# Optimization experiments

Measured on AMD Instinct MI355X. Metric: run time of the kernel, lower is better.

The kernel has to match this reference:

```python
import jax, jax.numpy as jnp
import numpy as np

B, S, D, E, K = 4, 4096, 2048, 64, 2


def setup_inputs() -> dict:
    key = jax.random.key(0)
    kx, kwg, kwn, kn = jax.random.split(key, 4)
    scale = 1.0 / np.sqrt(D)
    return {
        "x": jax.random.normal(kx, (B, S, D), dtype=jnp.float32),
        "Wg": jax.random.normal(kwg, (E, D), dtype=jnp.float32) * scale,
        "bg": jnp.zeros((E,), dtype=jnp.float32),
        "Wn": jax.random.normal(kwn, (E, D), dtype=jnp.float32) * scale,
        "bn": jnp.zeros((E,), dtype=jnp.float32),
        "noise": jax.random.normal(kn, (B, S, E), dtype=jnp.float32),
    }


def reference(x, Wg, bg, Wn, bn, noise):
    # gate / noise projections: [B,S,D] @ [D,E] -> [B,S,E]
    gate_logits = jnp.einsum("bsd,ed->bse", x, Wg) + bg
    noise_std = jax.nn.softplus(jnp.einsum("bsd,ed->bse", x, Wn) + bn)
    noisy_logits = gate_logits + noise * noise_std  # training-mode path

    # top-k over experts, then scatter back with -inf elsewhere
    flat = noisy_logits.reshape(-1, E)  # [T, E], T = B*S
    top_vals, top_idx = jax.lax.top_k(flat, K)  # [T, K]
    T = flat.shape[0]
    neg_inf = jnp.full((T, E), -jnp.inf, dtype=flat.dtype)
    full_logits = neg_inf.at[jnp.arange(T)[:, None], top_idx].set(top_vals)

    gate_probs = jax.nn.softmax(full_logits, axis=-1).reshape(B, S, E)
    top_k_indices = top_idx.reshape(B, S, K)
    return gate_probs, top_k_indices
```

## Files before the change

### kernel.cpp

```cpp
#include <hip/hip_runtime.h>
#include <math.h>
#include <stdint.h>

#define D_ 2048
#define E_ 64
#define T_ 16384

#define BM 32
#define BK 32
#define KTILES 64
#define ABUF_B 4096
#define BBUF_B 16384
#define BUF_B (ABUF_B + BBUF_B)
#define CT_STRIDE 132

typedef _Float16 h8 __attribute__((ext_vector_type(8)));
typedef float f4v __attribute__((ext_vector_type(4)));

__device__ __forceinline__ void split2(const float4& a, const float4& b,
                                       h8& h, h8& m) {
    const float xe[8] = {a.x, a.y, a.z, a.w, b.x, b.y, b.z, b.w};
#pragma unroll
    for (int i = 0; i < 8; ++i) {
        const _Float16 hh_ = (_Float16)xe[i];
        const float r = (xe[i] - (float)hh_) * 1024.0f;
        h[i] = hh_;
        m[i] = (_Float16)r;
    }
}

__device__ __forceinline__ void gload16(const void* g, void* l) {
    __builtin_amdgcn_global_load_lds(
        (const __attribute__((address_space(1))) uint32_t*)g,
        (__attribute__((address_space(3))) uint32_t*)l, 16, 0, 0);
}

__device__ __forceinline__ void topk_epilogue(float g, float nl, float nz,
                                              int lane, size_t tg,
                                              float* __restrict__ out_probs,
                                              float* __restrict__ out_idx) {
    const float sp = fmaxf(nl, 0.f) + log1pf(expf(-fabsf(nl)));
    const float noisy = g + nz * sp;

    float v = noisy;
    int idx = lane;
#pragma unroll
    for (int off = 32; off > 0; off >>= 1) {
        const float ov = __shfl_xor(v, off);
        const int oi = __shfl_xor(idx, off);
        if (ov > v || (ov == v && oi < idx)) { v = ov; idx = oi; }
    }
    const float v1 = v;
    const int i1 = idx;
    v = (lane == i1) ? -INFINITY : noisy;
    idx = lane;
#pragma unroll
    for (int off = 32; off > 0; off >>= 1) {
        const float ov = __shfl_xor(v, off);
        const int oi = __shfl_xor(idx, off);
        if (ov > v || (ov == v && oi < idx)) { v = ov; idx = oi; }
    }
    const float v2 = v;
    const int i2 = idx;

    const float e2 = expf(v2 - v1);
    const float denom = 1.f + e2;
    const float p = (lane == i1) ? (1.f / denom)
                                 : ((lane == i2) ? (e2 / denom) : 0.f);
    out_probs[tg * E_ + lane] = p;
    if (lane == 0) {
        out_idx[tg * 2 + 0] = (float)i1;
        out_idx[tg * 2 + 1] = (float)i2;
    }
}

__global__ void w_split_kernel(const float* __restrict__ Wg,
                               const float* __restrict__ Wn,
                               h8* __restrict__ wsp) {
    const int idx = blockIdx.x * blockDim.x + threadIdx.x;
    const int lane = idx & 63;
    const int s = (idx >> 6) & 63;
    const int f = idx >> 12;
    const int n = f * 16 + (lane & 15);
    const int k0 = s * 32 + ((lane >> 4) << 3);
    const float* src = (n < 64) ? &Wg[(size_t)n * D_ + k0]
                                : &Wn[(size_t)(n - 64) * D_ + k0];
    h8 hv, mv;
#pragma unroll
    for (int i = 0; i < 8; ++i) {
        const float w = src[i];
        const _Float16 wh = (_Float16)w;
        const float r = (w - (float)wh) * 1024.0f;
        hv[i] = wh;
        mv[i] = (_Float16)r;
    }
    wsp[0 * 32768 + idx] = hv;
    wsp[1 * 32768 + idx] = mv;
}

__launch_bounds__(512)
__global__ void gemm_topk_kernel(const float* __restrict__ x,
                                 const h8* __restrict__ wsp,
                                 const float* __restrict__ bg,
                                 const float* __restrict__ bn,
                                 const float* __restrict__ noise,
                                 float* __restrict__ out_probs,
                                 float* __restrict__ out_idx) {
    __shared__ __align__(16) char smem[2 * BUF_B];
    const int tid = threadIdx.x;
    const int lane = tid & 63;
    const int wv = tid >> 6;
    const int wm = wv >> 2;
    const int wn = wv & 3;
    const int block_m0 = blockIdx.x * BM;

    const int arow = lane & 15;
    const int akg = lane >> 4;
    const char* wb = (const char*)wsp;

    f4v hh0{}, hh1{}, hm0{}, hm1{}, mh0{}, mh1{}, mm0{}, mm1{};

    const int sar = tid >> 3;
    const int sac = tid & 7;
    const float* sasrc = x + (size_t)(block_m0 + sar) * D_ + ((sac ^ (sar & 7)) << 2);
    const int blv = lane;

    auto STAGE = [&](int t, int b) {
        char* base = smem + b * BUF_B;
        if (tid < 256)
            gload16(sasrc + t * BK, base + tid * 16);
        gload16(wb + ((size_t)(0 * 32768 + wv * 4096 + t * 64 + blv)) * 16,
                base + ABUF_B + ((0 * 8 + wv) * 64 + blv) * 16);
        gload16(wb + ((size_t)(1 * 32768 + wv * 4096 + t * 64 + blv)) * 16,
                base + ABUF_B + ((1 * 8 + wv) * 64 + blv) * 16);
    };

    auto COMPUTE = [&](int b) {
        const char* base = smem + b * BUF_B;
        const int r = wm * 16 + arow;
        const int swz = r & 7;
        const float4 f0 = *(const float4*)(base + r * 128 + (((akg * 2 + 0) ^ swz) << 4));
        const float4 f1 = *(const float4*)(base + r * 128 + (((akg * 2 + 1) ^ swz) << 4));
        h8 xh, xm;
        split2(f0, f1, xh, xm);
        const char* Bb = base + ABUF_B;
        const int fA = wn * 2, fB = wn * 2 + 1;
        const h8 bh0 = *(const h8*)(Bb + (fA * 64 + lane) * 16);
        const h8 bh1 = *(const h8*)(Bb + (fB * 64 + lane) * 16);
        const h8 bm0 = *(const h8*)(Bb + ((8 + fA) * 64 + lane) * 16);
        const h8 bm1 = *(const h8*)(Bb + ((8 + fB) * 64 + lane) * 16);
#define MF(A, B, C) C = __builtin_amdgcn_mfma_f32_16x16x32_f16(A, B, C, 0, 0, 0)
        MF(xh, bh0, hh0); MF(xh, bh1, hh1);
        MF(xh, bm0, hm0); MF(xh, bm1, hm1);
        MF(xm, bh0, mh0); MF(xm, bh1, mh1);
        MF(xm, bm0, mm0); MF(xm, bm1, mm1);
#undef MF
    };

    STAGE(0, 0);
    __syncthreads();
    int cur = 0;
#pragma unroll 1
    for (int t = 0; t < KTILES; ++t) {
        if (t + 1 < KTILES) STAGE(t + 1, cur ^ 1);
        COMPUTE(cur);
        __syncthreads();
        cur ^= 1;
    }

    float* Ct = (float*)smem;
    {
        const float S1 = 1.0f / 1024.0f;
        const float S2 = S1 * S1;
        const int ko4 = akg * 4;
#pragma unroll
        for (int r = 0; r < 4; ++r) {
            const int row = wm * 16 + ko4 + r;
            const int col0 = (wn * 2 + 0) * 16 + arow;
            const int col1 = (wn * 2 + 1) * 16 + arow;
            Ct[row * CT_STRIDE + col0] = hh0[r] + (hm0[r] + mh0[r]) * S1 + mm0[r] * S2;
            Ct[row * CT_STRIDE + col1] = hh1[r] + (hm1[r] + mh1[r]) * S1 + mm1[r] * S2;
        }
    }
    __syncthreads();

    const float my_bg = bg[lane];
    const float my_bn = bn[lane];
#pragma unroll 1
    for (int tt = 0; tt < 4; ++tt) {
        const int tl = wv * 4 + tt;
        const size_t tg = (size_t)block_m0 + tl;
        const float g = Ct[tl * CT_STRIDE + lane] + my_bg;
        const float nl = Ct[tl * CT_STRIDE + 64 + lane] + my_bn;
        const float nz = noise[tg * E_ + lane];
        topk_epilogue(g, nl, nz, lane, tg, out_probs, out_idx);
    }
}

#define FBM 64
#define FBK 32
#define XS_STRIDE 68
#define WS_STRIDE 132
#define FCT_STRIDE 132

__launch_bounds__(256)
__global__ void noisy_topk_f32_kernel(const float* __restrict__ x,
                                      const float* __restrict__ Wg,
                                      const float* __restrict__ bg,
                                      const float* __restrict__ Wn,
                                      const float* __restrict__ bn,
                                      const float* __restrict__ noise,
                                      float* __restrict__ out_probs,
                                      float* __restrict__ out_idx) {
    __shared__ float smem[FBM * FCT_STRIDE];
    float* Xs = smem;
    float* Ws = smem + FBK * XS_STRIDE;

    const int tid = threadIdx.x;
    const int block_m0 = blockIdx.x * FBM;
    const int n0 = (tid & 31) * 4;
    const int m0 = (tid >> 5) * 8;

    float acc[8][4];
#pragma unroll
    for (int i = 0; i < 8; ++i)
#pragma unroll
        for (int j = 0; j < 4; ++j) acc[i][j] = 0.f;

    const int sj = tid & 7;
    const int sr = tid >> 3;

    for (int k0 = 0; k0 < D_; k0 += FBK) {
        __syncthreads();
#pragma unroll
        for (int it = 0; it < 2; ++it) {
            const int m = sr + it * 32;
            const float4 v = *reinterpret_cast<const float4*>(
                &x[(size_t)(block_m0 + m) * D_ + k0 + 4 * sj]);
            Xs[(4 * sj + 0) * XS_STRIDE + m] = v.x;
            Xs[(4 * sj + 1) * XS_STRIDE + m] = v.y;
            Xs[(4 * sj + 2) * XS_STRIDE + m] = v.z;
            Xs[(4 * sj + 3) * XS_STRIDE + m] = v.w;
        }
#pragma unroll
        for (int it = 0; it < 4; ++it) {
            const int n = sr + it * 32;
            const float* wrow = (n < 64) ? &Wg[(size_t)n * D_] : &Wn[(size_t)(n - 64) * D_];
            const float4 v = *reinterpret_cast<const float4*>(&wrow[k0 + 4 * sj]);
            Ws[(4 * sj + 0) * WS_STRIDE + n] = v.x;
            Ws[(4 * sj + 1) * WS_STRIDE + n] = v.y;
            Ws[(4 * sj + 2) * WS_STRIDE + n] = v.z;
            Ws[(4 * sj + 3) * WS_STRIDE + n] = v.w;
        }
        __syncthreads();
#pragma unroll
        for (int k = 0; k < FBK; ++k) {
            const float4 a0 = *reinterpret_cast<const float4*>(&Xs[k * XS_STRIDE + m0]);
            const float4 a1 = *reinterpret_cast<const float4*>(&Xs[k * XS_STRIDE + m0 + 4]);
            const float4 b4 = *reinterpret_cast<const float4*>(&Ws[k * WS_STRIDE + n0]);
            const float am[8] = {a0.x, a0.y, a0.z, a0.w, a1.x, a1.y, a1.z, a1.w};
            const float bb[4] = {b4.x, b4.y, b4.z, b4.w};
#pragma unroll
            for (int i = 0; i < 8; ++i)
#pragma unroll
                for (int j = 0; j < 4; ++j)
                    acc[i][j] = fmaf(am[i], bb[j], acc[i][j]);
        }
    }

    __syncthreads();
    float* Ct = smem;
#pragma unroll
    for (int i = 0; i < 8; ++i)
#pragma unroll
        for (int j = 0; j < 4; ++j)
            Ct[(m0 + i) * FCT_STRIDE + n0 + j] = acc[i][j];
    __syncthreads();

    const int wave = tid >> 6;
    const int lane = tid & 63;
    const float my_bg = bg[lane];
    const float my_bn = bn[lane];
#pragma unroll 1
    for (int tt = 0; tt < 16; ++tt) {
        const int tl = wave * 16 + tt;
        const size_t tg = (size_t)block_m0 + tl;
        const float g = Ct[tl * FCT_STRIDE + lane] + my_bg;
        const float nl = Ct[tl * FCT_STRIDE + 64 + lane] + my_bn;
        const float nz = noise[tg * E_ + lane];
        topk_epilogue(g, nl, nz, lane, tg, out_probs, out_idx);
    }
}

extern "C" void kernel_launch(void* const* d_in, const int* in_sizes, int n_in,
                              void* d_out, int out_size, void* d_ws, size_t ws_size,
                              hipStream_t stream) {
    const float* x = (const float*)d_in[0];
    const float* Wg = (const float*)d_in[1];
    const float* bg = (const float*)d_in[2];
    const float* Wn = (const float*)d_in[3];
    const float* bn = (const float*)d_in[4];
    const float* noise = (const float*)d_in[5];
    float* out_probs = (float*)d_out;
    float* out_idx = out_probs + (size_t)T_ * E_;

    const size_t WSP_BYTES = (size_t)2 * 32768 * 16;
    if (ws_size >= WSP_BYTES) {
        h8* wsp = (h8*)d_ws;
        hipLaunchKernelGGL(w_split_kernel, dim3(128), dim3(256), 0, stream, Wg, Wn, wsp);
        hipLaunchKernelGGL(gemm_topk_kernel, dim3(T_ / BM), dim3(512), 0, stream,
                           x, wsp, bg, bn, noise, out_probs, out_idx);
    } else {
        hipLaunchKernelGGL(noisy_topk_f32_kernel, dim3(T_ / FBM), dim3(256), 0, stream,
                           x, Wg, bg, Wn, bn, noise, out_probs, out_idx);
    }
}
```

Baseline: 65.95 us.

## Enlarge GEMM tile to 64x64 and pre-split x into fp16 in LDS

Doubles the M and K tile sizes so each wave computes a 2x2 block of MFMA fragments, giving more reuse of the B operand per LDS read. Activations are now loaded into registers a tile ahead, split into high and low fp16 halves once per element, and stored to LDS in MFMA fragment order. This replaces the old scheme where every wave re-split raw floats read from LDS. The two cross-term MFMAs now accumulate into a single register, cutting accumulator count. In exchange the LDS footprint per block rises to about 96KB, which lowers occupancy, and the grid has half as many blocks.

```diff
diff --git a/kernel.cpp b/kernel.cpp
--- a/kernel.cpp
+++ b/kernel.cpp
@@ -6,11 +6,11 @@
 #define E_ 64
 #define T_ 16384
 
-#define BM 32
-#define BK 32
-#define KTILES 64
-#define ABUF_B 4096
-#define BBUF_B 16384
+#define BM 64
+#define BK 64
+#define KTILES 32
+#define ABUF_B 16384
+#define BBUF_B 32768
 #define BUF_B (ABUF_B + BBUF_B)
 #define CT_STRIDE 132
 
@@ -113,82 +113,119 @@
     const int wm = wv >> 2;
     const int wn = wv & 3;
     const int block_m0 = blockIdx.x * BM;
-
-    const int arow = lane & 15;
-    const int akg = lane >> 4;
     const char* wb = (const char*)wsp;
 
-    f4v hh0{}, hh1{}, hm0{}, hm1{}, mh0{}, mh1{}, mm0{}, mm1{};
-
-    const int sar = tid >> 3;
-    const int sac = tid & 7;
-    const float* sasrc = x + (size_t)(block_m0 + sar) * D_ + ((sac ^ (sar & 7)) << 2);
-    const int blv = lane;
-
-    auto STAGE = [&](int t, int b) {
-        char* base = smem + b * BUF_B;
-        if (tid < 256)
-            gload16(sasrc + t * BK, base + tid * 16);
-        gload16(wb + ((size_t)(0 * 32768 + wv * 4096 + t * 64 + blv)) * 16,
-                base + ABUF_B + ((0 * 8 + wv) * 64 + blv) * 16);
-        gload16(wb + ((size_t)(1 * 32768 + wv * 4096 + t * 64 + blv)) * 16,
-                base + ABUF_B + ((1 * 8 + wv) * 64 + blv) * 16);
+    const int sfrag = tid >> 7;
+    const int sks = (tid >> 6) & 1;
+    const int sl = tid & 63;
+    const int srow = sfrag * 16 + (sl & 15);
+    const int schunk = sks * 4 + (sl >> 4);
+    const float* asrc = x + (size_t)(block_m0 + srow) * D_ + schunk * 8;
+    const int aw_hi = ((0 * 4 + sfrag) * 2 + sks) * 1024 + sl * 16;
+    const int aw_mid = ((1 * 4 + sfrag) * 2 + sks) * 1024 + sl * 16;
+
+    f4v hh[2][2] = {}, cx[2][2] = {}, mm[2][2] = {};
+
+    auto STAGE_B = [&](int t, int b) {
+        char* Bb = smem + b * BUF_B + ABUF_B;
+#pragma unroll
+        for (int p = 0; p < 2; ++p)
+#pragma unroll
+            for (int ks = 0; ks < 2; ++ks)
+                gload16(wb + ((size_t)(p * 32768 + wv * 4096 + (t * 2 + ks) * 64 + lane)) * 16,
+                        Bb + ((p * 8 + wv) * 2 + ks) * 1024 + lane * 16);
     };
-
+    auto ALOAD = [&](int t, float4& ra, float4& rb) {
+        ra = *(const float4*)(asrc + t * BK);
+        rb = *(const float4*)(asrc + t * BK + 4);
+    };
+    auto ASPLIT = [&](const float4& ra, const float4& rb, int b) {
+        h8 hv, mv;
+        split2(ra, rb, hv, mv);
+        char* Ab = smem + b * BUF_B;
+        *(h8*)(Ab + aw_hi) = hv;
+        *(h8*)(Ab + aw_mid) = mv;
+    };
     auto COMPUTE = [&](int b) {
-        const char* base = smem + b * BUF_B;
-        const int r = wm * 16 + arow;
-        const int swz = r & 7;
-        const float4 f0 = *(const float4*)(base + r * 128 + (((akg * 2 + 0) ^ swz) << 4));
-        const float4 f1 = *(const float4*)(base + r * 128 + (((akg * 2 + 1) ^ swz) << 4));
-        h8 xh, xm;
-        split2(f0, f1, xh, xm);
-        const char* Bb = base + ABUF_B;
-        const int fA = wn * 2, fB = wn * 2 + 1;
-        const h8 bh0 = *(const h8*)(Bb + (fA * 64 + lane) * 16);
-        const h8 bh1 = *(const h8*)(Bb + (fB * 64 + lane) * 16);
-        const h8 bm0 = *(const h8*)(Bb + ((8 + fA) * 64 + lane) * 16);
-        const h8 bm1 = *(const h8*)(Bb + ((8 + fB) * 64 + lane) * 16);
+        const char* Ab = smem + b * BUF_B;
+        const char* Bb = Ab + ABUF_B;
+#pragma unroll
+        for (int ks = 0; ks < 2; ++ks) {
+            h8 ah[2], am[2], bh[2], bm[2];
+#pragma unroll
+            for (int mi = 0; mi < 2; ++mi) {
+                const int mf = wm * 2 + mi;
+                ah[mi] = *(const h8*)(Ab + ((0 * 4 + mf) * 2 + ks) * 1024 + lane * 16);
+                am[mi] = *(const h8*)(Ab + ((1 * 4 + mf) * 2 + ks) * 1024 + lane * 16);
+            }
+#pragma unroll
+            for (int nf = 0; nf < 2; ++nf) {
+                const int f = wn * 2 + nf;
+                bh[nf] = *(const h8*)(Bb + ((0 * 8 + f) * 2 + ks) * 1024 + lane * 16);
+                bm[nf] = *(const h8*)(Bb + ((1 * 8 + f) * 2 + ks) * 1024 + lane * 16);
+            }
 #define MF(A, B, C) C = __builtin_amdgcn_mfma_f32_16x16x32_f16(A, B, C, 0, 0, 0)
-        MF(xh, bh0, hh0); MF(xh, bh1, hh1);
-        MF(xh, bm0, hm0); MF(xh, bm1, hm1);
-        MF(xm, bh0, mh0); MF(xm, bh1, mh1);
-        MF(xm, bm0, mm0); MF(xm, bm1, mm1);
+#pragma unroll
+            for (int mi = 0; mi < 2; ++mi)
+#pragma unroll
+                for (int nf = 0; nf < 2; ++nf) {
+                    MF(ah[mi], bh[nf], hh[mi][nf]);
+                    MF(ah[mi], bm[nf], cx[mi][nf]);
+                    MF(am[mi], bh[nf], cx[mi][nf]);
+                    MF(am[mi], bm[nf], mm[mi][nf]);
+                }
 #undef MF
+        }
     };
 
-    STAGE(0, 0);
+    float4 ra0, rb0, ra1, rb1;
+    ALOAD(0, ra0, rb0);
+    STAGE_B(0, 0);
+    ASPLIT(ra0, rb0, 0);
+    ALOAD(1, ra0, rb0);
     __syncthreads();
-    int cur = 0;
+
 #pragma unroll 1
-    for (int t = 0; t < KTILES; ++t) {
-        if (t + 1 < KTILES) STAGE(t + 1, cur ^ 1);
-        COMPUTE(cur);
+    for (int i = 0; i < KTILES / 2; ++i) {
+        const int t = 2 * i;
+        STAGE_B(t + 1, 1);
+        if (t + 2 < KTILES) ALOAD(t + 2, ra1, rb1);
+        COMPUTE(0);
+        ASPLIT(ra0, rb0, 1);
         __syncthreads();
-        cur ^= 1;
+        if (t + 2 < KTILES) STAGE_B(t + 2, 0);
+        if (t + 3 < KTILES) ALOAD(t + 3, ra0, rb0);
+        COMPUTE(1);
+        if (t + 2 < KTILES) ASPLIT(ra1, rb1, 0);
+        __syncthreads();
     }
 
     float* Ct = (float*)smem;
     {
         const float S1 = 1.0f / 1024.0f;
         const float S2 = S1 * S1;
-        const int ko4 = akg * 4;
-#pragma unroll
-        for (int r = 0; r < 4; ++r) {
-            const int row = wm * 16 + ko4 + r;
-            const int col0 = (wn * 2 + 0) * 16 + arow;
-            const int col1 = (wn * 2 + 1) * 16 + arow;
-            Ct[row * CT_STRIDE + col0] = hh0[r] + (hm0[r] + mh0[r]) * S1 + mm0[r] * S2;
-            Ct[row * CT_STRIDE + col1] = hh1[r] + (hm1[r] + mh1[r]) * S1 + mm1[r] * S2;
-        }
+        const int arow = lane & 15;
+        const int ko4 = (lane >> 4) * 4;
+#pragma unroll
+        for (int mi = 0; mi < 2; ++mi)
+#pragma unroll
+            for (int nf = 0; nf < 2; ++nf) {
+                const int col = wn * 32 + nf * 16 + arow;
+#pragma unroll
+                for (int r = 0; r < 4; ++r) {
+                    const int row = wm * 32 + mi * 16 + ko4 + r;
+                    Ct[row * CT_STRIDE + col] =
+                        hh[mi][nf][r] + cx[mi][nf][r] * S1 + mm[mi][nf][r] * S2;
+                }
+            }
     }
     __syncthreads();
 
     const float my_bg = bg[lane];
     const float my_bn = bn[lane];
 #pragma unroll 1
-    for (int tt = 0; tt < 4; ++tt) {
-        const int tl = wv * 4 + tt;
+    for (int tt = 0; tt < 8; ++tt) {
+        const int tl = wv * 8 + tt;
         const size_t tg = (size_t)block_m0 + tl;
         const float g = Ct[tl * CT_STRIDE + lane] + my_bg;
         const float nl = Ct[tl * CT_STRIDE + 64 + lane] + my_bn;
```

After: 59.62 us. 9.6% less time.

## Replace LDS double-buffered staging with direct register prefetch in GEMM-topk

Applied to the files above, without the earlier changes.

Removes the shared-memory staging of x and the split weights, along with the per-step barrier. Each wave now loads its A fragment and B fragments straight from global memory into registers, with two steps of software prefetch. The two cross-term accumulators are merged into one, which frees registers, and launch bounds now request 4 blocks per CU. The trade-off is that x rows are read without the coalescing that LDS staging gave, and each wave refetches the weights from cache itself instead of sharing one block-wide copy.

```diff
diff --git a/kernel.cpp b/kernel.cpp
--- a/kernel.cpp
+++ b/kernel.cpp
@@ -7,11 +7,7 @@
 #define T_ 16384
 
 #define BM 32
-#define BK 32
-#define KTILES 64
-#define ABUF_B 4096
-#define BBUF_B 16384
-#define BUF_B (ABUF_B + BBUF_B)
+#define NSTEP 64
 #define CT_STRIDE 132
 
 typedef _Float16 h8 __attribute__((ext_vector_type(8)));
@@ -27,12 +23,6 @@
         h[i] = hh_;
         m[i] = (_Float16)r;
     }
-}
-
-__device__ __forceinline__ void gload16(const void* g, void* l) {
-    __builtin_amdgcn_global_load_lds(
-        (const __attribute__((address_space(1))) uint32_t*)g,
-        (__attribute__((address_space(3))) uint32_t*)l, 16, 0, 0);
 }
 
 __device__ __forceinline__ void topk_epilogue(float g, float nl, float nz,
@@ -98,7 +88,7 @@
     wsp[1 * 32768 + idx] = mv;
 }
 
-__launch_bounds__(512)
+__launch_bounds__(512, 4)
 __global__ void gemm_topk_kernel(const float* __restrict__ x,
                                  const h8* __restrict__ wsp,
                                  const float* __restrict__ bg,
@@ -106,7 +96,7 @@
                                  const float* __restrict__ noise,
                                  float* __restrict__ out_probs,
                                  float* __restrict__ out_idx) {
-    __shared__ __align__(16) char smem[2 * BUF_B];
+    __shared__ float Ct[BM * CT_STRIDE];
     const int tid = threadIdx.x;
     const int lane = tid & 63;
     const int wv = tid >> 6;
@@ -116,59 +106,56 @@
 
     const int arow = lane & 15;
     const int akg = lane >> 4;
-    const char* wb = (const char*)wsp;
-
-    f4v hh0{}, hh1{}, hm0{}, hm1{}, mh0{}, mh1{}, mm0{}, mm1{};
-
-    const int sar = tid >> 3;
-    const int sac = tid & 7;
-    const float* sasrc = x + (size_t)(block_m0 + sar) * D_ + ((sac ^ (sar & 7)) << 2);
-    const int blv = lane;
-
-    auto STAGE = [&](int t, int b) {
-        char* base = smem + b * BUF_B;
-        if (tid < 256)
-            gload16(sasrc + t * BK, base + tid * 16);
-        gload16(wb + ((size_t)(0 * 32768 + wv * 4096 + t * 64 + blv)) * 16,
-                base + ABUF_B + ((0 * 8 + wv) * 64 + blv) * 16);
-        gload16(wb + ((size_t)(1 * 32768 + wv * 4096 + t * 64 + blv)) * 16,
-                base + ABUF_B + ((1 * 8 + wv) * 64 + blv) * 16);
-    };
-
-    auto COMPUTE = [&](int b) {
-        const char* base = smem + b * BUF_B;
-        const int r = wm * 16 + arow;
-        const int swz = r & 7;
-        const float4 f0 = *(const float4*)(base + r * 128 + (((akg * 2 + 0) ^ swz) << 4));
-        const float4 f1 = *(const float4*)(base + r * 128 + (((akg * 2 + 1) ^ swz) << 4));
-        h8 xh, xm;
-        split2(f0, f1, xh, xm);
-        const char* Bb = base + ABUF_B;
-        const int fA = wn * 2, fB = wn * 2 + 1;
-        const h8 bh0 = *(const h8*)(Bb + (fA * 64 + lane) * 16);
-        const h8 bh1 = *(const h8*)(Bb + (fB * 64 + lane) * 16);
-        const h8 bm0 = *(const h8*)(Bb + ((8 + fA) * 64 + lane) * 16);
-        const h8 bm1 = *(const h8*)(Bb + ((8 + fB) * 64 + lane) * 16);
+
+    const float* xp = x + (size_t)(block_m0 + wm * 16 + arow) * D_ + akg * 8;
+    const int fA = wn * 2, fB = wn * 2 + 1;
+    const h8* pb0 = wsp + 0 * 32768 + fA * 4096 + lane;
+    const h8* pb1 = wsp + 0 * 32768 + fB * 4096 + lane;
+    const h8* pb2 = wsp + 1 * 32768 + fA * 4096 + lane;
+    const h8* pb3 = wsp + 1 * 32768 + fB * 4096 + lane;
+
+    f4v hh0{}, hh1{}, cx0{}, cx1{}, mm0{}, mm1{};
+
+#define ALOADR(t, ra, rb)                                        \
+    ra = *(const float4*)(xp + (t) * 32);                        \
+    rb = *(const float4*)(xp + (t) * 32 + 4);
+#define BLOADR(t, b0, b1, b2, b3)                                \
+    b0 = pb0[(t) * 64]; b1 = pb1[(t) * 64];                      \
+    b2 = pb2[(t) * 64]; b3 = pb3[(t) * 64];
 #define MF(A, B, C) C = __builtin_amdgcn_mfma_f32_16x16x32_f16(A, B, C, 0, 0, 0)
-        MF(xh, bh0, hh0); MF(xh, bh1, hh1);
-        MF(xh, bm0, hm0); MF(xh, bm1, hm1);
-        MF(xm, bh0, mh0); MF(xm, bh1, mh1);
-        MF(xm, bm0, mm0); MF(xm, bm1, mm1);
+#define STEP_MFMA(xh, xm, b0, b1, b2, b3)                        \
+    MF(xh, b0, hh0); MF(xh, b1, hh1);                            \
+    MF(xh, b2, cx0); MF(xh, b3, cx1);                            \
+    MF(xm, b0, cx0); MF(xm, b1, cx1);                            \
+    MF(xm, b2, mm0); MF(xm, b3, mm1);
+
+    float4 aA0, aA1, aB0, aB1;
+    h8 pA0, pA1, pA2, pA3, pB0, pB1, pB2, pB3;
+    ALOADR(0, aA0, aA1); BLOADR(0, pA0, pA1, pA2, pA3);
+    ALOADR(1, aB0, aB1); BLOADR(1, pB0, pB1, pB2, pB3);
+
+#pragma unroll 1
+    for (int t = 0; t < NSTEP; t += 2) {
+        {
+            h8 xh, xm;
+            split2(aA0, aA1, xh, xm);
+            const h8 b0 = pA0, b1 = pA1, b2 = pA2, b3 = pA3;
+            if (t + 2 < NSTEP) { ALOADR(t + 2, aA0, aA1); BLOADR(t + 2, pA0, pA1, pA2, pA3); }
+            STEP_MFMA(xh, xm, b0, b1, b2, b3)
+        }
+        {
+            h8 xh, xm;
+            split2(aB0, aB1, xh, xm);
+            const h8 b0 = pB0, b1 = pB1, b2 = pB2, b3 = pB3;
+            if (t + 3 < NSTEP) { ALOADR(t + 3, aB0, aB1); BLOADR(t + 3, pB0, pB1, pB2, pB3); }
+            STEP_MFMA(xh, xm, b0, b1, b2, b3)
+        }
+    }
+#undef STEP_MFMA
 #undef MF
-    };
-
-    STAGE(0, 0);
-    __syncthreads();
-    int cur = 0;
-#pragma unroll 1
-    for (int t = 0; t < KTILES; ++t) {
-        if (t + 1 < KTILES) STAGE(t + 1, cur ^ 1);
-        COMPUTE(cur);
-        __syncthreads();
-        cur ^= 1;
-    }
-
-    float* Ct = (float*)smem;
+#undef BLOADR
+#undef ALOADR
+
     {
         const float S1 = 1.0f / 1024.0f;
         const float S2 = S1 * S1;
@@ -176,10 +163,10 @@
 #pragma unroll
         for (int r = 0; r < 4; ++r) {
             const int row = wm * 16 + ko4 + r;
-            const int col0 = (wn * 2 + 0) * 16 + arow;
-            const int col1 = (wn * 2 + 1) * 16 + arow;
-            Ct[row * CT_STRIDE + col0] = hh0[r] + (hm0[r] + mh0[r]) * S1 + mm0[r] * S2;
-            Ct[row * CT_STRIDE + col1] = hh1[r] + (hm1[r] + mh1[r]) * S1 + mm1[r] * S2;
+            Ct[row * CT_STRIDE + wn * 32 + 0 * 16 + arow] =
+                hh0[r] + cx0[r] * S1 + mm0[r] * S2;
+            Ct[row * CT_STRIDE + wn * 32 + 1 * 16 + arow] =
+                hh1[r] + cx1[r] * S1 + mm1[r] * S2;
         }
     }
     __syncthreads();
```

New measurement: 107.3 us. 1.63x slower.
